# Kernel optimization log

Hardware: AMD Instinct MI355X
Metric: run time of the kernel (lower is better)

## Reference

```python
import jax, jax.numpy as jnp
import numpy as np

NX, NY, C, B, P = 432, 496, 64, 4, 40000


def setup_inputs() -> dict:
    key = jax.random.key(0)
    k1, _ = jax.random.split(key)
    pillar_features = jax.random.normal(k1, (P, C), dtype=jnp.float32)
    # Build voxel_coords with unique (x, y) cells per batch element so the
    # scatter-write has no duplicate indices (matches deterministic torch assignment).
    rng = np.random.default_rng(0)
    per = P // B  # pillars per sample
    coords = np.empty((P, 3), dtype=np.int64)
    for b in range(B):
        flat = rng.choice(NX * NY, size=per, replace=False)
        coords[b * per:(b + 1) * per, 0] = flat % NX          # x index
        coords[b * per:(b + 1) * per, 1] = flat // NX         # y index
        coords[b * per:(b + 1) * per, 2] = b                  # batch index (last col)
    return {
        "pillar_features": pillar_features,
        "voxel_coords": jnp.asarray(coords),
        "batch_size": B,
        "nx": NX,
        "ny": NY,
    }


def reference(pillar_features, voxel_coords, batch_size, nx, ny):
    # Fused scatter: compute a global flat index (batch, y, x) for every pillar
    # and scatter all pillars in a single pass (no per-batch masking loop).
    x = voxel_coords[:, 0]
    y = voxel_coords[:, 1]
    b = voxel_coords[:, -1]
    flat = b * (ny * nx) + y * nx + x                       # [P]
    c = pillar_features.shape[1]
    grid = jnp.zeros((batch_size * ny * nx, c), dtype=pillar_features.dtype)
    grid = grid.at[flat].set(pillar_features)               # scatter pillars
    # [B*ny*nx, C] -> [B, C, ny, nx]
    return grid.reshape(batch_size, ny, nx, c).transpose(0, 3, 1, 2)
```

## Files before the change

kernel.cpp:

```cpp
#include <hip/hip_runtime.h>


#define C_CH 64

typedef float nat_float4 __attribute__((ext_vector_type(4)));

__global__ void build_map_kernel(const int* __restrict__ coords, int n_pillars,
                                 const int* __restrict__ nx_p,
                                 const int* __restrict__ ny_p,
                                 int* __restrict__ map) {
    int p = blockIdx.x * blockDim.x + threadIdx.x;
    if (p >= n_pillars) return;
    const int nx = nx_p[0];
    const int ny = ny_p[0];
    const int x = coords[3 * p + 0];
    const int y = coords[3 * p + 1];
    const int b = coords[3 * p + 2];
    const long long m = (long long)b * (long long)(nx * ny) + (long long)y * nx + x;
    map[m] = p;
}

__global__ void __launch_bounds__(256) gather64x4_kernel(
        const float* __restrict__ feat,
        const int* __restrict__ map,
        const int* __restrict__ nx_p,
        const int* __restrict__ ny_p,
        float* __restrict__ out, int n_cell4) {
    const int t = blockIdx.x * blockDim.x + threadIdx.x;
    if (t >= n_cell4) return;
    const int plane4 = (nx_p[0] * ny_p[0]) >> 2;
    const int b = t / plane4;
    const int rem4 = t - b * plane4;

    const int4 pv = ((const int4*)map)[t];

    const float* __restrict__ f0 = feat + (long long)pv.x * C_CH;
    const float* __restrict__ f1 = feat + (long long)pv.y * C_CH;
    const float* __restrict__ f2 = feat + (long long)pv.z * C_CH;
    const float* __restrict__ f3 = feat + (long long)pv.w * C_CH;

    nat_float4* __restrict__ out4 = (nat_float4*)out;
    const int base = b * C_CH * plane4 + rem4;

#pragma unroll 8
    for (int c = 0; c < C_CH; ++c) {
        nat_float4 v = {0.f, 0.f, 0.f, 0.f};
        if (pv.x >= 0) v.x = f0[c];
        if (pv.y >= 0) v.y = f1[c];
        if (pv.z >= 0) v.z = f2[c];
        if (pv.w >= 0) v.w = f3[c];
        __builtin_nontemporal_store(v, out4 + base + c * plane4);
    }
}

__global__ void direct_scatter_kernel(const float* __restrict__ feat,
                                      const int* __restrict__ coords,
                                      int n_pillars, int C,
                                      const int* __restrict__ nx_p,
                                      const int* __restrict__ ny_p,
                                      float* __restrict__ out) {
    const long long t = (long long)blockIdx.x * blockDim.x + threadIdx.x;
    if (t >= (long long)n_pillars * C) return;
    const int p = (int)(t / C);
    const int c = (int)(t - (long long)p * C);
    const int nx = nx_p[0];
    const int ny = ny_p[0];
    const int x = coords[3 * p + 0];
    const int y = coords[3 * p + 1];
    const int b = coords[3 * p + 2];
    const int plane = nx * ny;
    const size_t o = ((size_t)b * C + c) * (size_t)plane + (size_t)y * nx + x;
    out[o] = feat[(size_t)p * C + c];
}

extern "C" void kernel_launch(void* const* d_in, const int* in_sizes, int n_in,
                              void* d_out, int out_size, void* d_ws, size_t ws_size,
                              hipStream_t stream) {
    const float* feat   = (const float*)d_in[0];
    const int*   coords = (const int*)d_in[1];
    const int* nx_p = (const int*)d_in[3];
    const int* ny_p = (const int*)d_in[4];
    float* out = (float*)d_out;

    const int n_pillars = in_sizes[1] / 3;
    const int C = in_sizes[0] / n_pillars;
    const int n_map = out_size / C;
    const size_t map_bytes = (size_t)n_map * sizeof(int);

    if (C == C_CH && (n_map & 3) == 0 && ws_size >= map_bytes) {
        int* map = (int*)d_ws;
        (void)hipMemsetAsync(map, 0xFF, map_bytes, stream);
        build_map_kernel<<<(n_pillars + 255) / 256, 256, 0, stream>>>(
            coords, n_pillars, nx_p, ny_p, map);
        const int n_cell4 = n_map >> 2;
        gather64x4_kernel<<<(n_cell4 + 255) / 256, 256, 0, stream>>>(
            feat, map, nx_p, ny_p, out, n_cell4);
    } else {
        (void)hipMemsetAsync(out, 0, (size_t)out_size * sizeof(float), stream);
        const long long total = (long long)n_pillars * C;
        direct_scatter_kernel<<<(unsigned)((total + 255) / 256), 256, 0, stream>>>(
            feat, coords, n_pillars, C, nx_p, ny_p, out);
    }
}
```

Before: 242.1 us.

## Parallelize gather over output float4s instead of looping channels per thread

Each thread now produces one float4 of the output, decoding batch, channel and spatial position from its linear index, instead of looping over all 64 channels for a group of four cells. This gives 64x more threads with contiguous, fully coalesced stores and no per-thread serial loop, aiming for better latency hiding. In exchange the map is re-read once per channel (64x map traffic, mostly cache hits), and feature reads become strided gathers across channels.

```diff
diff --git a/kernel.cpp b/kernel.cpp
--- a/kernel.cpp
+++ b/kernel.cpp
@@ -20,37 +20,30 @@
     map[m] = p;
 }
 
-__global__ void __launch_bounds__(256) gather64x4_kernel(
+__global__ void __launch_bounds__(256) gather_linear_kernel(
         const float* __restrict__ feat,
         const int* __restrict__ map,
         const int* __restrict__ nx_p,
         const int* __restrict__ ny_p,
-        float* __restrict__ out, int n_cell4) {
+        float* __restrict__ out, int n_out4) {
     const int t = blockIdx.x * blockDim.x + threadIdx.x;
-    if (t >= n_cell4) return;
+    if (t >= n_out4) return;
     const int plane4 = (nx_p[0] * ny_p[0]) >> 2;
-    const int b = t / plane4;
-    const int rem4 = t - b * plane4;
 
-    const int4 pv = ((const int4*)map)[t];
+    const int bc  = t / plane4;
+    const int yx4 = t - bc * plane4;
+    const int b   = bc >> 6;
+    const int c   = bc & 63;
 
-    const float* __restrict__ f0 = feat + (long long)pv.x * C_CH;
-    const float* __restrict__ f1 = feat + (long long)pv.y * C_CH;
-    const float* __restrict__ f2 = feat + (long long)pv.z * C_CH;
-    const float* __restrict__ f3 = feat + (long long)pv.w * C_CH;
+    const int4 pv = ((const int4*)map)[b * plane4 + yx4];
 
-    nat_float4* __restrict__ out4 = (nat_float4*)out;
-    const int base = b * C_CH * plane4 + rem4;
+    nat_float4 v = {0.f, 0.f, 0.f, 0.f};
+    if (pv.x >= 0) v.x = feat[pv.x * C_CH + c];
+    if (pv.y >= 0) v.y = feat[pv.y * C_CH + c];
+    if (pv.z >= 0) v.z = feat[pv.z * C_CH + c];
+    if (pv.w >= 0) v.w = feat[pv.w * C_CH + c];
 
-#pragma unroll 8
-    for (int c = 0; c < C_CH; ++c) {
-        nat_float4 v = {0.f, 0.f, 0.f, 0.f};
-        if (pv.x >= 0) v.x = f0[c];
-        if (pv.y >= 0) v.y = f1[c];
-        if (pv.z >= 0) v.z = f2[c];
-        if (pv.w >= 0) v.w = f3[c];
-        __builtin_nontemporal_store(v, out4 + base + c * plane4);
-    }
+    __builtin_nontemporal_store(v, ((nat_float4*)out) + t);
 }
 
 __global__ void direct_scatter_kernel(const float* __restrict__ feat,
@@ -87,14 +80,15 @@
     const int n_map = out_size / C;
     const size_t map_bytes = (size_t)n_map * sizeof(int);
 
-    if (C == C_CH && (n_map & 3) == 0 && ws_size >= map_bytes) {
+    if (C == C_CH && (n_map & 3) == 0 && (out_size & 3) == 0 &&
+        ws_size >= map_bytes) {
         int* map = (int*)d_ws;
         (void)hipMemsetAsync(map, 0xFF, map_bytes, stream);
         build_map_kernel<<<(n_pillars + 255) / 256, 256, 0, stream>>>(
             coords, n_pillars, nx_p, ny_p, map);
-        const int n_cell4 = n_map >> 2;
-        gather64x4_kernel<<<(n_cell4 + 255) / 256, 256, 0, stream>>>(
-            feat, map, nx_p, ny_p, out, n_cell4);
+        const int n_out4 = out_size >> 2;
+        gather_linear_kernel<<<(n_out4 + 255) / 256, 256, 0, stream>>>(
+            feat, map, nx_p, ny_p, out, n_out4);
     } else {
         (void)hipMemsetAsync(out, 0, (size_t)out_size * sizeof(float), stream);
         const long long total = (long long)n_pillars * C;
```

Measured after the change: 242.4 us. No clear change (+0.1%).
